# Optimization experiments

Hardware: AMD Instinct MI355X
Metric: run time of the kernel (lower is better)

## Reference

```python
import jax, jax.numpy as jnp
import numpy as np

B, N, F = 8, 1024, 64
H, C = 4, 32              # attention heads, channels per head
HIN = H * C               # GAT output size (concat heads) = 128
HID = 128                 # GRU hidden size
NEG_INF = -1e9


def _glorot(key, shape, fan_in, fan_out):
    scale = np.sqrt(2.0 / (fan_in + fan_out)).astype(np.float32)
    return jax.random.normal(key, shape, jnp.float32) * scale


def setup_inputs() -> dict:
    key = jax.random.key(0)
    ks = jax.random.split(key, 20)
    x = jax.random.normal(ks[0], (B, N, F), jnp.float32)
    a = (jax.random.uniform(ks[1], (B, N, N)) < 0.01).astype(jnp.float32)
    h = jax.random.normal(ks[2], (B, N, HID), jnp.float32) * 0.1
    # GATConv params (spektral dense mode, concat heads)
    Wk = _glorot(ks[3], (F, H, C), F, H * C)
    att_src = _glorot(ks[4], (H, C), C, 1)
    att_dst = _glorot(ks[5], (H, C), C, 1)
    bias_gat = jnp.zeros((HIN,), jnp.float32)
    # GRU-style gates (per-node biases, concat weights)
    b_u = _glorot(ks[6], (N, 1), N, 1)
    b_r = _glorot(ks[7], (N, 1), N, 1)
    b_c = _glorot(ks[8], (N, 1), N, 1)
    W_u = _glorot(ks[9], (HID + HIN, HID), HID + HIN, HID)
    W_r = _glorot(ks[10], (HID + HIN, HID), HID + HIN, HID)
    W_c = _glorot(ks[11], (HID + HIN, HID), HID + HIN, HID)
    # bilinear decoders
    R_p = _glorot(ks[12], (HID, HID), HID, HID)
    R_mu = _glorot(ks[13], (HID, HID), HID, HID)
    R_sigma = _glorot(ks[14], (HID, HID), HID, HID)
    return {"x": x, "a": a, "h": h, "Wk": Wk, "att_src": att_src,
            "att_dst": att_dst, "bias_gat": bias_gat,
            "b_u": b_u, "b_r": b_r, "b_c": b_c,
            "W_u": W_u, "W_r": W_r, "W_c": W_c,
            "R_p": R_p, "R_mu": R_mu, "R_sigma": R_sigma}


def reference(x, a, h, Wk, att_src, att_dst, bias_gat,
              b_u, b_r, b_c, W_u, W_r, W_c, R_p, R_mu, R_sigma):
    # ---- GATConv (dense mode, concat heads) ----
    hh = jnp.einsum('bnf,fhc->bnhc', x, Wk)                 # [B,N,H,C]
    s_src = jnp.einsum('bnhc,hc->bnh', hh, att_src)         # per-node src score
    s_dst = jnp.einsum('bnhc,hc->bnh', hh, att_dst)         # per-node dst score
    e = jax.nn.leaky_relu(s_src[:, :, None, :] + s_dst[:, None, :, :], 0.2)  # [B,N,N,H]
    e = e + NEG_INF * (1.0 - a)[..., None]                  # mask non-edges
    attn = jax.nn.softmax(e, axis=2)                        # softmax over neighbors j
    conv = jnp.einsum('bijh,bjhc->bihc', attn, hh)          # neighbor aggregation
    conv = conv.reshape(B, N, HIN) + bias_gat               # concat heads + bias
    # ---- GRU-style gated update ----
    cu = jnp.concatenate([conv, h], axis=-1)                # [B,N,HIN+HID]
    u = jax.nn.sigmoid(b_u + cu @ W_u)
    r = jax.nn.sigmoid(b_r + cu @ W_r)
    c = jnp.tanh(b_c + jnp.concatenate([conv, r * h], axis=-1) @ W_c)
    h_prime = u * h + (1.0 - u) * c                         # [B,N,HID]
    # dropout is identity at inference (training=False)
    # ---- three bilinear decoders ----
    def dec(R):
        return jnp.einsum('bnh,hk,bmk->bnm', h_prime, R, h_prime)
    logits = jnp.stack([dec(R_p), dec(R_mu), dec(R_sigma)], axis=-1)  # [B,N,N,3]
    return (logits, h_prime)
```

## Files before the change

kernel.cpp:

```cpp
#include <hip/hip_runtime.h>

#define BB 8
#define NNODES 1024
#define FIN 64
#define NH 4
#define NC 32
#define HDIM 128
#define NEG_INF_F (-1e9f)

#define LOGITS_CNT (BB*NNODES*NNODES*3)
#define HP_OFF LOGITS_CNT

#define CP1_OFF  (2*BB*NNODES*HDIM)
#define HHTB_OFF (3*BB*NNODES*HDIM)
#define WT_OFF   (4*BB*NNODES*HDIM)
#define RT_OFF   (WT_OFF + 49152)

#define WS_HH    0
#define WS_SSRC  (WS_HH    + BB*NNODES*HDIM)
#define WS_SDSTT (WS_SSRC  + BB*NNODES*NH)
#define WS_M     (WS_SDSTT + BB*NH*NNODES)
#define WS_RSUM  (WS_M     + BB*NNODES*NH)
#define WS_CONV  (WS_RSUM  + BB*NNODES*NH)
#define WS_T     (WS_CONV  + BB*NNODES*HDIM)
#define HPB_FOFF (WS_T + 1572864)

typedef float f32x4 __attribute__((ext_vector_type(4)));
typedef short bf16x8 __attribute__((ext_vector_type(8)));

__device__ __forceinline__ float sigmoidf_(float x) { return 1.0f/(1.0f+__expf(-x)); }
__device__ __forceinline__ float tanhf_(float x) {
  float e = __expf(2.0f*x); return 1.0f - 2.0f/(e+1.0f);
}
__device__ __forceinline__ void ld4(const float* p, float* d) {
  float4 v = *(const float4*)p;
  d[0]=v.x; d[1]=v.y; d[2]=v.z; d[3]=v.w;
}
__device__ __forceinline__ ushort f2b(float x) {
  union { float f; unsigned u; } v; v.f = x;
  unsigned r = v.u + 0x7fffu + ((v.u >> 16) & 1u);
  return (ushort)(r >> 16);
}

__global__ __launch_bounds__(256) void k_prep(
    const float* __restrict__ W_u, const float* __restrict__ W_r,
    const float* __restrict__ W_c, const float* __restrict__ R_p,
    const float* __restrict__ R_mu, const float* __restrict__ R_sg,
    float* __restrict__ out)
{
  __shared__ float tile[64*129];
  int blk = blockIdx.x, tid = threadIdx.x;
  const float* src; ushort* dst; int k0, nk;
  if (blk < 12) {
    int mat = blk >> 2, ch = blk & 3; k0 = ch*64; nk = 256;
    src = (mat==0) ? W_u : (mat==1) ? W_r : W_c;
    dst = (ushort*)(out + WT_OFF) + mat*32768;
  } else {
    int q = blk - 12; int mat = q >> 1, ch = q & 1; k0 = ch*64; nk = 128;
    src = (mat==0) ? R_p : (mat==1) ? R_mu : R_sg;
    dst = (ushort*)(out + RT_OFF) + mat*16384;
  }
  #pragma unroll
  for (int t = 0; t < 8; ++t) {
    int g = tid + t*256;
    int r = g >> 5, c4 = g & 31;
    *(float4*)&tile[r*129 + c4*4] = *(const float4*)&src[(size_t)(k0+r)*HDIM + c4*4];
  }
  __syncthreads();
  int c = tid >> 1, half = tid & 1;
  ushort tmp[32];
  #pragma unroll
  for (int q = 0; q < 32; ++q) tmp[q] = f2b(tile[(half*32+q)*129 + c]);
  size_t base = (size_t)c*nk + k0 + half*32;
  #pragma unroll
  for (int g = 0; g < 4; ++g) {
    uint4 v;
    v.x = (uint)tmp[g*8+0] | ((uint)tmp[g*8+1] << 16);
    v.y = (uint)tmp[g*8+2] | ((uint)tmp[g*8+3] << 16);
    v.z = (uint)tmp[g*8+4] | ((uint)tmp[g*8+5] << 16);
    v.w = (uint)tmp[g*8+6] | ((uint)tmp[g*8+7] << 16);
    *(uint4*)&dst[base + g*8] = v;
  }
}

#define XK_S 68
#define HT2_S 129
__global__ __launch_bounds__(256) void k_hh_scores(
    const float* __restrict__ x, const float* __restrict__ Wk,
    const float* __restrict__ att_src, const float* __restrict__ att_dst,
    float* __restrict__ ws, float* __restrict__ out)
{
  __shared__ union {
    struct { float wk[FIN*HDIM]; float x[32*XK_S]; } s;
    float hhT[32*HT2_S];
  } u;
  int tid = threadIdx.x;
  int blk = blockIdx.x;
  int b = blk >> 5;
  int n0 = (blk & 31) * 32;
  #pragma unroll
  for (int t = 0; t < 8; ++t) {
    int idx = tid + t*256;
    int r = idx >> 5, c4 = idx & 31;
    *(float4*)&u.s.wk[r*HDIM + c4*4] = *(const float4*)&Wk[r*HDIM + c4*4];
  }
  #pragma unroll
  for (int t = 0; t < 2; ++t) {
    int idx = tid + t*256;
    int r = idx >> 4, c4 = idx & 15;
    *(float4*)&u.s.x[r*XK_S + c4*4] =
      *(const float4*)&x[((size_t)(b*NNODES)+n0+r)*FIN + c4*4];
  }
  __syncthreads();
  int col = tid & 127;
  int rh = tid >> 7;
  float acc[16];
  #pragma unroll
  for (int rr = 0; rr < 16; ++rr) acc[rr] = 0.f;
  for (int k4 = 0; k4 < 16; ++k4) {
    float w0 = u.s.wk[(k4*4+0)*HDIM + col];
    float w1 = u.s.wk[(k4*4+1)*HDIM + col];
    float w2 = u.s.wk[(k4*4+2)*HDIM + col];
    float w3 = u.s.wk[(k4*4+3)*HDIM + col];
    #pragma unroll
    for (int rr = 0; rr < 16; ++rr) {
      float4 xv = *(const float4*)&u.s.x[(rh*16+rr)*XK_S + k4*4];
      acc[rr] = fmaf(xv.x, w0, fmaf(xv.y, w1, fmaf(xv.z, w2, fmaf(xv.w, w3, acc[rr]))));
    }
  }
  {
    float as = att_src[col], ad = att_dst[col];
    float* ssrc  = ws + WS_SSRC;
    float* sdstT = ws + WS_SDSTT;
    int hI = col >> 5;
    #pragma unroll
    for (int rr = 0; rr < 16; ++rr) {
      int n = n0 + rh*16 + rr;
      float ss = acc[rr]*as, sd = acc[rr]*ad;
      #pragma unroll
      for (int m = 16; m >= 1; m >>= 1) {
        ss += __shfl_xor(ss, m, 64);
        sd += __shfl_xor(sd, m, 64);
      }
      if ((col & 31) == 0) {
        ssrc[((size_t)(b*NNODES)+n)*NH + hI] = ss;
        sdstT[(size_t)(b*NH + hI)*NNODES + n] = sd;
      }
    }
  }
  __syncthreads();
  #pragma unroll
  for (int rr = 0; rr < 16; ++rr)
    u.hhT[(rh*16+rr)*HT2_S + col] = acc[rr];
  __syncthreads();
  {
    ushort* HHTB = (ushort*)(out + HHTB_OFF);
    int c = tid >> 1, half = tid & 1;
    ushort tmp[16];
    #pragma unroll
    for (int q = 0; q < 16; ++q)
      tmp[q] = f2b(u.hhT[(half*16+q)*HT2_S + c]);
    size_t base = ((size_t)(b*HDIM)+c)*NNODES + n0 + half*16;
    #pragma unroll
    for (int g = 0; g < 2; ++g) {
      uint4 v;
      v.x = (uint)tmp[g*8+0] | ((uint)tmp[g*8+1] << 16);
      v.y = (uint)tmp[g*8+2] | ((uint)tmp[g*8+3] << 16);
      v.z = (uint)tmp[g*8+4] | ((uint)tmp[g*8+5] << 16);
      v.w = (uint)tmp[g*8+6] | ((uint)tmp[g*8+7] << 16);
      *(uint4*)&HHTB[base + g*8] = v;
    }
  }
}

__global__ __launch_bounds__(256) void k_stats(
    const float* __restrict__ a, float* __restrict__ ws)
{
  __shared__ float a_l[NNODES];
  int tid = threadIdx.x;
  int blk = blockIdx.x;
  int b = blk & 7, i = blk >> 3;
  const float* arow = a + ((size_t)(b*NNODES + i))*NNODES;
  *(float4*)&a_l[tid*4] = *(const float4*)&arow[tid*4];
  __syncthreads();
  int h = tid >> 6, lane = tid & 63;
  const float* ssrc  = ws + WS_SSRC;
  const float* sdstT = ws + WS_SDSTT;
  float si = ssrc[((size_t)(b*NNODES)+i)*NH + h];
  float e[16];
  float mx = -3.4e38f;
  #pragma unroll
  for (int t = 0; t < 16; ++t) {
    int j = lane + t*64;
    float s = si + sdstT[(size_t)(b*NH+h)*NNODES + j];
    float ev = s >= 0.f ? s : 0.2f*s;
    ev += NEG_INF_F * (1.0f - a_l[j]);
    e[t] = ev;
    mx = fmaxf(mx, ev);
  }
  #pragma unroll
  for (int m = 32; m >= 1; m >>= 1) mx = fmaxf(mx, __shfl_xor(mx, m, 64));
  float sum = 0.f;
  #pragma unroll
  for (int t = 0; t < 16; ++t) sum += __expf(e[t] - mx);
  #pragma unroll
  for (int m = 32; m >= 1; m >>= 1) sum += __shfl_xor(sum, m, 64);
  if (lane == 0) {
    ws[WS_M    + ((size_t)(b*NNODES)+i)*NH + h] = mx;
    ws[WS_RSUM + ((size_t)(b*NNODES)+i)*NH + h] = 1.0f / sum;
  }
}

#define HT_S 40
__global__ __launch_bounds__(256) void k_conv_m(
    const float* __restrict__ a,
    float* __restrict__ ws, float* __restrict__ out)
{
  __shared__ ushort hhT_l[128*HT_S];
  __shared__ float sdst_l[4*32];
  int tid = threadIdx.x;
  int blk = blockIdx.x;
  int b = blk & 7;
  int rem = blk >> 3;
  int it = rem >> 1, jh = rem & 1;
  int i0 = it * 32;
  int j0b = jh * 512;
  int w = tid >> 6, lane = tid & 63;
  int i0w = i0 + (w & 1) * 16;
  int hp2 = (w >> 1) * 2;
  int i = i0w + (lane & 15);
  int koff = (lane >> 4) * 8;
  const ushort* HHTB = (const ushort*)(out + HHTB_OFF);
  const float* sdstT = ws + WS_SDSTT;
  float ssv[4], mv[4], rsv[4];
  ld4(&ws[WS_SSRC + ((size_t)(b*NNODES)+i)*4], ssv);
  ld4(&ws[WS_M    + ((size_t)(b*NNODES)+i)*4], mv);
  ld4(&ws[WS_RSUM + ((size_t)(b*NNODES)+i)*4], rsv);
  f32x4 acc[2][2];
  #pragma unroll
  for (int h = 0; h < 2; ++h)
    #pragma unroll
    for (int cf = 0; cf < 2; ++cf) acc[h][cf] = (f32x4)0.f;
  const float* arow = a + ((size_t)(b*NNODES)+i)*NNODES;
  for (int ch = 0; ch < 16; ++ch) {
    int j0 = j0b + ch*32;
    #pragma unroll
    for (int s = 0; s < 2; ++s) {
      int seg = tid + s*256;
      int c = seg >> 2, q = seg & 3;
      *(uint4*)&hhT_l[c*HT_S + q*8] =
        *(const uint4*)&HHTB[((size_t)(b*HDIM)+c)*NNODES + j0 + q*8];
    }
    if (tid < 32) {
      int h = tid >> 3, q = tid & 7;
      *(float4*)&sdst_l[h*32 + q*4] =
        *(const float4*)&sdstT[(size_t)(b*NH + h)*NNODES + j0 + q*4];
    }
    float av[8];
    {
      float4 a0 = *(const float4*)&arow[j0 + koff];
      float4 a1 = *(const float4*)&arow[j0 + koff + 4];
      av[0]=a0.x; av[1]=a0.y; av[2]=a0.z; av[3]=a0.w;
      av[4]=a1.x; av[5]=a1.y; av[6]=a1.z; av[7]=a1.w;
    }
    __syncthreads();
    float am[8];
    #pragma unroll
    for (int t = 0; t < 8; ++t) am[t] = fmaf(av[t], 1e9f, -1e9f);
    #pragma unroll
    for (int h2 = 0; h2 < 2; ++h2) {
      int hh_ = hp2 + h2;
      float sd[8];
      ld4(&sdst_l[hh_*32 + koff], sd);
      ld4(&sdst_l[hh_*32 + koff + 4], sd + 4);
      bf16x8 pf;
      #pragma unroll
      for (int t = 0; t < 8; ++t) {
        float s = ssv[hh_] + sd[t];
        s = fmaxf(s, 0.2f*s);
        float p = __expf(s + am[t] - mv[hh_]) * rsv[hh_];
        pf[t] = (short)f2b(p);
      }
      #pragma unroll
      for (int cf = 0; cf < 2; ++cf) {
        int c = hh_*32 + cf*16 + (lane & 15);
        bf16x8 bfr = *(const bf16x8*)&hhT_l[c*HT_S + koff];
        acc[h2][cf] = __builtin_amdgcn_mfma_f32_16x16x32_bf16(
            pf, bfr, acc[h2][cf], 0, 0, 0);
      }
    }
    __syncthreads();
  }
  float* cp = jh ? (out + CP1_OFF) : (ws + WS_CONV);
  int crow = (lane >> 4) * 4, ccol = lane & 15;
  #pragma unroll
  for (int h2 = 0; h2 < 2; ++h2)
    #pragma unroll
    for (int cf = 0; cf < 2; ++cf)
      #pragma unroll
      for (int r = 0; r < 4; ++r)
        cp[((size_t)(b*NNODES) + i0w + crow + r)*HDIM + (hp2+h2)*32 + cf*16 + ccol]
          = acc[h2][cf][r];
}

#define CU_S 264
#define RH_S 136
__global__ __launch_bounds__(256) void k_fuse(
    const float* __restrict__ h_in,
    const float* __restrict__ b_u, const float* __restrict__ b_r,
    const float* __restrict__ b_c, const float* __restrict__ bias_gat,
    float* __restrict__ ws, float* __restrict__ out)
{
  __shared__ ushort cu_l[16*CU_S];
  __shared__ ushort rh_l[16*RH_S];
  __shared__ ushort hp_l[16*RH_S];
  int tid = threadIdx.x;
  int blk = blockIdx.x;
  int b = blk & 7;
  int n0 = (blk >> 3) * 16;
  const float* conv0 = ws + WS_CONV;
  const float* conv1 = out + CP1_OFF;
  const ushort* WT = (const ushort*)(out + WT_OFF);
  const ushort* RT = (const ushort*)(out + RT_OFF);
  ushort* HPB = (ushort*)(ws + HPB_FOFF);
  ushort* TB  = (ushort*)(ws + WS_T);
  #pragma unroll
  for (int t = 0; t < 4; ++t) {
    int g = tid + t*256;
    int row = g >> 6, c4 = g & 63;
    float v[4];
    if (c4 < 32) {
      float4 v0 = *(const float4*)&conv0[((size_t)(b*NNODES)+n0+row)*HDIM + c4*4];
      float4 v1 = *(const float4*)&conv1[((size_t)(b*NNODES)+n0+row)*HDIM + c4*4];
      float4 bv = *(const float4*)&bias_gat[c4*4];
      v[0]=v0.x+v1.x+bv.x; v[1]=v0.y+v1.y+bv.y; v[2]=v0.z+v1.z+bv.z; v[3]=v0.w+v1.w+bv.w;
    } else {
      ld4(&h_in[((size_t)(b*NNODES)+n0+row)*HDIM + (c4-32)*4], v);
    }
    ushort4 o; o.x=f2b(v[0]); o.y=f2b(v[1]); o.z=f2b(v[2]); o.w=f2b(v[3]);
    *(ushort4*)&cu_l[row*CU_S + c4*4] = o;
  }
  __syncthreads();
  int w = tid >> 6, lane = tid & 63;
  int wn = w * 32;
  int fr = lane & 15, k8 = (lane >> 4) * 8;
  int crow = (lane >> 4) * 4, ccol = lane & 15;
  f32x4 acc_u[2], acc_r[2];
  acc_u[0]=(f32x4)0.f; acc_u[1]=(f32x4)0.f; acc_r[0]=(f32x4)0.f; acc_r[1]=(f32x4)0.f;
  #pragma unroll
  for (int ks = 0; ks < 8; ++ks) {
    bf16x8 afr = *(const bf16x8*)&cu_l[fr*CU_S + ks*32 + k8];
    #pragma unroll
    for (int nn = 0; nn < 2; ++nn) {
      int row = wn + nn*16 + fr;
      bf16x8 bu_ = *(const bf16x8*)&WT[(size_t)row*256 + ks*32 + k8];
      bf16x8 br_ = *(const bf16x8*)&WT[32768 + (size_t)row*256 + ks*32 + k8];
      acc_u[nn] = __builtin_amdgcn_mfma_f32_16x16x32_bf16(afr, bu_, acc_u[nn], 0,0,0);
      acc_r[nn] = __builtin_amdgcn_mfma_f32_16x16x32_bf16(afr, br_, acc_r[nn], 0,0,0);
    }
  }
  float u_reg[2][4], hv[2][4];
  float bu4[4], br4[4], bc4[4];
  #pragma unroll
  for (int r = 0; r < 4; ++r) {
    bu4[r] = b_u[n0 + crow + r];
    br4[r] = b_r[n0 + crow + r];
    bc4[r] = b_c[n0 + crow + r];
  }
  #pragma unroll
  for (int nn = 0; nn < 2; ++nn) {
    int col = wn + nn*16 + ccol;
    #pragma unroll
    for (int r = 0; r < 4; ++r) {
      int rown = crow + r;
      float h_ = h_in[((size_t)(b*NNODES)+n0+rown)*HDIM + col];
      hv[nn][r] = h_;
      u_reg[nn][r] = sigmoidf_(bu4[r] + acc_u[nn][r]);
      float rr_ = sigmoidf_(br4[r] + acc_r[nn][r]);
      rh_l[rown*RH_S + col] = f2b(rr_ * h_);
    }
  }
  __syncthreads();
  f32x4 acc_c[2];
  acc_c[0]=(f32x4)0.f; acc_c[1]=(f32x4)0.f;
  #pragma unroll
  for (int ks = 0; ks < 8; ++ks) {
    bf16x8 afr = (ks < 4)
      ? *(const bf16x8*)&cu_l[fr*CU_S + ks*32 + k8]
      : *(const bf16x8*)&rh_l[fr*RH_S + (ks-4)*32 + k8];
    #pragma unroll
    for (int nn = 0; nn < 2; ++nn) {
      int row = wn + nn*16 + fr;
      bf16x8 bc_ = *(const bf16x8*)&WT[65536 + (size_t)row*256 + ks*32 + k8];
      acc_c[nn] = __builtin_amdgcn_mfma_f32_16x16x32_bf16(afr, bc_, acc_c[nn], 0,0,0);
    }
  }
  #pragma unroll
  for (int nn = 0; nn < 2; ++nn) {
    int col = wn + nn*16 + ccol;
    #pragma unroll
    for (int r = 0; r < 4; ++r) {
      int rown = crow + r;
      float cc = tanhf_(bc4[r] + acc_c[nn][r]);
      float u_ = u_reg[nn][r];
      float hp = u_*hv[nn][r] + (1.0f-u_)*cc;
      out[HP_OFF + ((size_t)(b*NNODES)+n0+rown)*HDIM + col] = hp;
      ushort hb = f2b(hp);
      HPB[((size_t)(b*NNODES)+n0+rown)*HDIM + col] = hb;
      hp_l[rown*RH_S + col] = hb;
    }
  }
  __syncthreads();
  #pragma unroll
  for (int k3 = 0; k3 < 3; ++k3) {
    f32x4 acc_t[2];
    acc_t[0]=(f32x4)0.f; acc_t[1]=(f32x4)0.f;
    #pragma unroll
    for (int ks = 0; ks < 4; ++ks) {
      bf16x8 afr = *(const bf16x8*)&hp_l[fr*RH_S + ks*32 + k8];
      #pragma unroll
      for (int nn = 0; nn < 2; ++nn) {
        int row = wn + nn*16 + fr;
        bf16x8 bfr = *(const bf16x8*)&RT[k3*16384 + (size_t)row*128 + ks*32 + k8];
        acc_t[nn] = __builtin_amdgcn_mfma_f32_16x16x32_bf16(afr, bfr, acc_t[nn], 0,0,0);
      }
    }
    #pragma unroll
    for (int nn = 0; nn < 2; ++nn) {
      int col = wn + nn*16 + ccol;
      #pragma unroll
      for (int r = 0; r < 4; ++r)
        TB[((size_t)((b*3+k3)*NNODES)+n0+crow+r)*HDIM + col] = f2b(acc_t[nn][r]);
    }
  }
}

#define LT_S 136
__global__ __launch_bounds__(256) void k_logits_m(
    const float* __restrict__ ws, float* __restrict__ out)
{
  __shared__ ushort t_b[3][64*LT_S];
  __shared__ ushort hp_b[64*LT_S];
  const ushort* TB  = (const ushort*)(ws + WS_T);
  const ushort* HPB = (const ushort*)(ws + HPB_FOFF);
  int tid = threadIdx.x;
  int blk = blockIdx.x;
  int b = blk & 7;
  int rem = blk >> 3;
  int nt = rem >> 4, mt = rem & 15;
  int n0 = nt*64, m0 = mt*64;
  #pragma unroll
  for (int t = 0; t < 4; ++t) {
    int idx = tid + t*256;
    int r = idx >> 4, c = idx & 15;
    *(uint4*)&hp_b[r*LT_S + c*8] =
      *(const uint4*)&HPB[((size_t)(b*NNODES)+m0+r)*HDIM + c*8];
  }
  #pragma unroll
  for (int t = 0; t < 12; ++t) {
    int idx = tid + t*256;
    int k3 = idx >> 10, r = (idx >> 4) & 63, c = idx & 15;
    *(uint4*)&t_b[k3][r*LT_S + c*8] =
      *(const uint4*)&TB[((size_t)((b*3+k3)*NNODES)+n0+r)*HDIM + c*8];
  }
  __syncthreads();
  int w = tid >> 6, lane = tid & 63;
  int nbase = (w >> 1) * 32, mbase = (w & 1) * 32;
  int frow = lane & 15, fk = (lane >> 4) * 8;
  f32x4 acc[3][2][2];
  #pragma unroll
  for (int k3 = 0; k3 < 3; ++k3)
    #pragma unroll
    for (int nn = 0; nn < 2; ++nn)
      #pragma unroll
      for (int mm = 0; mm < 2; ++mm) acc[k3][nn][mm] = (f32x4)0.f;
  #pragma unroll
  for (int ks = 0; ks < 4; ++ks) {
    int ko = ks*32 + fk;
    bf16x8 bfr[2];
    #pragma unroll
    for (int mm = 0; mm < 2; ++mm)
      bfr[mm] = *(const bf16x8*)&hp_b[(mbase + mm*16 + frow)*LT_S + ko];
    #pragma unroll
    for (int k3 = 0; k3 < 3; ++k3)
      #pragma unroll
      for (int nn = 0; nn < 2; ++nn) {
        bf16x8 afr = *(const bf16x8*)&t_b[k3][(nbase + nn*16 + frow)*LT_S + ko];
        #pragma unroll
        for (int mm = 0; mm < 2; ++mm)
          acc[k3][nn][mm] = __builtin_amdgcn_mfma_f32_16x16x32_bf16(
              afr, bfr[mm], acc[k3][nn][mm], 0, 0, 0);
      }
  }
  int crow = (lane >> 4) * 4, ccol = lane & 15;
  #pragma unroll
  for (int nn = 0; nn < 2; ++nn)
    #pragma unroll
    for (int mm = 0; mm < 2; ++mm)
      #pragma unroll
      for (int r = 0; r < 4; ++r) {
        int n = n0 + nbase + nn*16 + crow + r;
        int m = m0 + mbase + mm*16 + ccol;
        float* po = &out[(((size_t)(b*NNODES) + n)*NNODES + m)*3];
        po[0] = acc[0][nn][mm][r];
        po[1] = acc[1][nn][mm][r];
        po[2] = acc[2][nn][mm][r];
      }
}

extern "C" void kernel_launch(void* const* d_in, const int* in_sizes, int n_in,
                              void* d_out, int out_size, void* d_ws, size_t ws_size,
                              hipStream_t stream) {
  (void)in_sizes; (void)n_in; (void)out_size; (void)ws_size;
  const float* x        = (const float*)d_in[0];
  const float* a        = (const float*)d_in[1];
  const float* h        = (const float*)d_in[2];
  const float* Wk       = (const float*)d_in[3];
  const float* att_src  = (const float*)d_in[4];
  const float* att_dst  = (const float*)d_in[5];
  const float* bias_gat = (const float*)d_in[6];
  const float* b_u      = (const float*)d_in[7];
  const float* b_r      = (const float*)d_in[8];
  const float* b_c      = (const float*)d_in[9];
  const float* W_u      = (const float*)d_in[10];
  const float* W_r      = (const float*)d_in[11];
  const float* W_c      = (const float*)d_in[12];
  const float* R_p      = (const float*)d_in[13];
  const float* R_mu     = (const float*)d_in[14];
  const float* R_sg     = (const float*)d_in[15];
  float* out = (float*)d_out;
  float* ws  = (float*)d_ws;

  hipLaunchKernelGGL(k_prep, dim3(18), dim3(256), 0, stream,
                     W_u, W_r, W_c, R_p, R_mu, R_sg, out);
  hipLaunchKernelGGL(k_hh_scores, dim3(256), dim3(256), 0, stream,
                     x, Wk, att_src, att_dst, ws, out);
  hipLaunchKernelGGL(k_stats, dim3(8192), dim3(256), 0, stream, a, ws);
  hipLaunchKernelGGL(k_conv_m, dim3(512), dim3(256), 0, stream, a, ws, out);
  hipLaunchKernelGGL(k_fuse, dim3(512), dim3(256), 0, stream,
                     h, b_u, b_r, b_c, bias_gat, ws, out);
  hipLaunchKernelGGL(k_logits_m, dim3(2048), dim3(256), 0, stream, ws, out);
}
```

Measured before the change: 100.7 us.

## Replace separate softmax stats pass with online softmax in conv kernel

Removes the k_stats kernel, which re-read the full adjacency matrix to compute per-row max and sum. k_conv_m now keeps a running max and sum per half of the neighbours (flash-attention style) and rescales its accumulators. k_fuse merges the two halves using the stored stats. The weight prep and hh/score kernels are also merged into one launch. This cuts a full pass over the adjacency and one launch, at the cost of extra exp, shuffles and rescaling inside the conv loop.

```diff
diff --git a/kernel.cpp b/kernel.cpp
--- a/kernel.cpp
+++ b/kernel.cpp
@@ -17,6 +17,8 @@
 #define RT_OFF   (WT_OFF + 49152)
 
 #define WS_HH    0
+#define WS_STATM WS_HH
+#define WS_STATS (WS_HH + 65536)
 #define WS_SSRC  (WS_HH    + BB*NNODES*HDIM)
 #define WS_SDSTT (WS_SSRC  + BB*NNODES*NH)
 #define WS_M     (WS_SDSTT + BB*NH*NNODES)
@@ -42,73 +44,70 @@
   return (ushort)(r >> 16);
 }
 
-__global__ __launch_bounds__(256) void k_prep(
+#define XK_S 68
+#define HT2_S 129
+__global__ __launch_bounds__(256) void k_pre(
+    const float* __restrict__ x, const float* __restrict__ Wk,
+    const float* __restrict__ att_src, const float* __restrict__ att_dst,
     const float* __restrict__ W_u, const float* __restrict__ W_r,
     const float* __restrict__ W_c, const float* __restrict__ R_p,
     const float* __restrict__ R_mu, const float* __restrict__ R_sg,
-    float* __restrict__ out)
-{
-  __shared__ float tile[64*129];
-  int blk = blockIdx.x, tid = threadIdx.x;
-  const float* src; ushort* dst; int k0, nk;
-  if (blk < 12) {
-    int mat = blk >> 2, ch = blk & 3; k0 = ch*64; nk = 256;
-    src = (mat==0) ? W_u : (mat==1) ? W_r : W_c;
-    dst = (ushort*)(out + WT_OFF) + mat*32768;
-  } else {
-    int q = blk - 12; int mat = q >> 1, ch = q & 1; k0 = ch*64; nk = 128;
-    src = (mat==0) ? R_p : (mat==1) ? R_mu : R_sg;
-    dst = (ushort*)(out + RT_OFF) + mat*16384;
-  }
-  #pragma unroll
-  for (int t = 0; t < 8; ++t) {
-    int g = tid + t*256;
-    int r = g >> 5, c4 = g & 31;
-    *(float4*)&tile[r*129 + c4*4] = *(const float4*)&src[(size_t)(k0+r)*HDIM + c4*4];
-  }
-  __syncthreads();
-  int c = tid >> 1, half = tid & 1;
-  ushort tmp[32];
-  #pragma unroll
-  for (int q = 0; q < 32; ++q) tmp[q] = f2b(tile[(half*32+q)*129 + c]);
-  size_t base = (size_t)c*nk + k0 + half*32;
-  #pragma unroll
-  for (int g = 0; g < 4; ++g) {
-    uint4 v;
-    v.x = (uint)tmp[g*8+0] | ((uint)tmp[g*8+1] << 16);
-    v.y = (uint)tmp[g*8+2] | ((uint)tmp[g*8+3] << 16);
-    v.z = (uint)tmp[g*8+4] | ((uint)tmp[g*8+5] << 16);
-    v.w = (uint)tmp[g*8+6] | ((uint)tmp[g*8+7] << 16);
-    *(uint4*)&dst[base + g*8] = v;
-  }
-}
-
-#define XK_S 68
-#define HT2_S 129
-__global__ __launch_bounds__(256) void k_hh_scores(
-    const float* __restrict__ x, const float* __restrict__ Wk,
-    const float* __restrict__ att_src, const float* __restrict__ att_dst,
     float* __restrict__ ws, float* __restrict__ out)
 {
-  __shared__ union {
-    struct { float wk[FIN*HDIM]; float x[32*XK_S]; } s;
-    float hhT[32*HT2_S];
-  } u;
-  int tid = threadIdx.x;
-  int blk = blockIdx.x;
-  int b = blk >> 5;
-  int n0 = (blk & 31) * 32;
+  __shared__ float sm[FIN*HDIM + 32*XK_S];
+  int blk = blockIdx.x, tid = threadIdx.x;
+  if (blk < 18) {
+    float* tile = sm;
+    const float* src; ushort* dst; int k0, nk;
+    if (blk < 12) {
+      int mat = blk >> 2, ch = blk & 3; k0 = ch*64; nk = 256;
+      src = (mat==0) ? W_u : (mat==1) ? W_r : W_c;
+      dst = (ushort*)(out + WT_OFF) + mat*32768;
+    } else {
+      int q = blk - 12; int mat = q >> 1, ch = q & 1; k0 = ch*64; nk = 128;
+      src = (mat==0) ? R_p : (mat==1) ? R_mu : R_sg;
+      dst = (ushort*)(out + RT_OFF) + mat*16384;
+    }
+    #pragma unroll
+    for (int t = 0; t < 8; ++t) {
+      int g = tid + t*256;
+      int r = g >> 5, c4 = g & 31;
+      *(float4*)&tile[r*129 + c4*4] = *(const float4*)&src[(size_t)(k0+r)*HDIM + c4*4];
+    }
+    __syncthreads();
+    int c = tid >> 1, half = tid & 1;
+    ushort tmp[32];
+    #pragma unroll
+    for (int q = 0; q < 32; ++q) tmp[q] = f2b(tile[(half*32+q)*129 + c]);
+    size_t base = (size_t)c*nk + k0 + half*32;
+    #pragma unroll
+    for (int g = 0; g < 4; ++g) {
+      uint4 v;
+      v.x = (uint)tmp[g*8+0] | ((uint)tmp[g*8+1] << 16);
+      v.y = (uint)tmp[g*8+2] | ((uint)tmp[g*8+3] << 16);
+      v.z = (uint)tmp[g*8+4] | ((uint)tmp[g*8+5] << 16);
+      v.w = (uint)tmp[g*8+6] | ((uint)tmp[g*8+7] << 16);
+      *(uint4*)&dst[base + g*8] = v;
+    }
+    return;
+  }
+  int blk2 = blk - 18;
+  int b = blk2 >> 5;
+  int n0 = (blk2 & 31) * 32;
+  float* wk_l = sm;
+  float* x_l  = sm + FIN*HDIM;
+  float* hhT  = sm;
   #pragma unroll
   for (int t = 0; t < 8; ++t) {
     int idx = tid + t*256;
     int r = idx >> 5, c4 = idx & 31;
-    *(float4*)&u.s.wk[r*HDIM + c4*4] = *(const float4*)&Wk[r*HDIM + c4*4];
+    *(float4*)&wk_l[r*HDIM + c4*4] = *(const float4*)&Wk[r*HDIM + c4*4];
   }
   #pragma unroll
   for (int t = 0; t < 2; ++t) {
     int idx = tid + t*256;
     int r = idx >> 4, c4 = idx & 15;
-    *(float4*)&u.s.x[r*XK_S + c4*4] =
+    *(float4*)&x_l[r*XK_S + c4*4] =
       *(const float4*)&x[((size_t)(b*NNODES)+n0+r)*FIN + c4*4];
   }
   __syncthreads();
@@ -118,13 +117,13 @@
   #pragma unroll
   for (int rr = 0; rr < 16; ++rr) acc[rr] = 0.f;
   for (int k4 = 0; k4 < 16; ++k4) {
-    float w0 = u.s.wk[(k4*4+0)*HDIM + col];
-    float w1 = u.s.wk[(k4*4+1)*HDIM + col];
-    float w2 = u.s.wk[(k4*4+2)*HDIM + col];
-    float w3 = u.s.wk[(k4*4+3)*HDIM + col];
+    float w0 = wk_l[(k4*4+0)*HDIM + col];
+    float w1 = wk_l[(k4*4+1)*HDIM + col];
+    float w2 = wk_l[(k4*4+2)*HDIM + col];
+    float w3 = wk_l[(k4*4+3)*HDIM + col];
     #pragma unroll
     for (int rr = 0; rr < 16; ++rr) {
-      float4 xv = *(const float4*)&u.s.x[(rh*16+rr)*XK_S + k4*4];
+      float4 xv = *(const float4*)&x_l[(rh*16+rr)*XK_S + k4*4];
       acc[rr] = fmaf(xv.x, w0, fmaf(xv.y, w1, fmaf(xv.z, w2, fmaf(xv.w, w3, acc[rr]))));
     }
   }
@@ -151,7 +150,7 @@
   __syncthreads();
   #pragma unroll
   for (int rr = 0; rr < 16; ++rr)
-    u.hhT[(rh*16+rr)*HT2_S + col] = acc[rr];
+    hhT[(rh*16+rr)*HT2_S + col] = acc[rr];
   __syncthreads();
   {
     ushort* HHTB = (ushort*)(out + HHTB_OFF);
@@ -159,7 +158,7 @@
     ushort tmp[16];
     #pragma unroll
     for (int q = 0; q < 16; ++q)
-      tmp[q] = f2b(u.hhT[(half*16+q)*HT2_S + c]);
+      tmp[q] = f2b(hhT[(half*16+q)*HT2_S + c]);
     size_t base = ((size_t)(b*HDIM)+c)*NNODES + n0 + half*16;
     #pragma unroll
     for (int g = 0; g < 2; ++g) {
@@ -170,44 +169,6 @@
       v.w = (uint)tmp[g*8+6] | ((uint)tmp[g*8+7] << 16);
       *(uint4*)&HHTB[base + g*8] = v;
     }
-  }
-}
-
-__global__ __launch_bounds__(256) void k_stats(
-    const float* __restrict__ a, float* __restrict__ ws)
-{
-  __shared__ float a_l[NNODES];
-  int tid = threadIdx.x;
-  int blk = blockIdx.x;
-  int b = blk & 7, i = blk >> 3;
-  const float* arow = a + ((size_t)(b*NNODES + i))*NNODES;
-  *(float4*)&a_l[tid*4] = *(const float4*)&arow[tid*4];
-  __syncthreads();
-  int h = tid >> 6, lane = tid & 63;
-  const float* ssrc  = ws + WS_SSRC;
-  const float* sdstT = ws + WS_SDSTT;
-  float si = ssrc[((size_t)(b*NNODES)+i)*NH + h];
-  float e[16];
-  float mx = -3.4e38f;
-  #pragma unroll
-  for (int t = 0; t < 16; ++t) {
-    int j = lane + t*64;
-    float s = si + sdstT[(size_t)(b*NH+h)*NNODES + j];
-    float ev = s >= 0.f ? s : 0.2f*s;
-    ev += NEG_INF_F * (1.0f - a_l[j]);
-    e[t] = ev;
-    mx = fmaxf(mx, ev);
-  }
-  #pragma unroll
-  for (int m = 32; m >= 1; m >>= 1) mx = fmaxf(mx, __shfl_xor(mx, m, 64));
-  float sum = 0.f;
-  #pragma unroll
-  for (int t = 0; t < 16; ++t) sum += __expf(e[t] - mx);
-  #pragma unroll
-  for (int m = 32; m >= 1; m >>= 1) sum += __shfl_xor(sum, m, 64);
-  if (lane == 0) {
-    ws[WS_M    + ((size_t)(b*NNODES)+i)*NH + h] = mx;
-    ws[WS_RSUM + ((size_t)(b*NNODES)+i)*NH + h] = 1.0f / sum;
   }
 }
 
@@ -228,14 +189,16 @@
   int w = tid >> 6, lane = tid & 63;
   int i0w = i0 + (w & 1) * 16;
   int hp2 = (w >> 1) * 2;
-  int i = i0w + (lane & 15);
+  int fr = lane & 15;
+  int i = i0w + fr;
   int koff = (lane >> 4) * 8;
+  int crow = (lane >> 4) * 4, ccol = lane & 15;
   const ushort* HHTB = (const ushort*)(out + HHTB_OFF);
   const float* sdstT = ws + WS_SDSTT;
-  float ssv[4], mv[4], rsv[4];
+  float ssv[4];
   ld4(&ws[WS_SSRC + ((size_t)(b*NNODES)+i)*4], ssv);
-  ld4(&ws[WS_M    + ((size_t)(b*NNODES)+i)*4], mv);
-  ld4(&ws[WS_RSUM + ((size_t)(b*NNODES)+i)*4], rsv);
+  float m_run[2] = {-3.0e38f, -3.0e38f};
+  float s_run[2] = {0.f, 0.f};
   f32x4 acc[2][2];
   #pragma unroll
   for (int h = 0; h < 2; ++h)
@@ -273,16 +236,38 @@
       float sd[8];
       ld4(&sdst_l[hh_*32 + koff], sd);
       ld4(&sdst_l[hh_*32 + koff + 4], sd + 4);
-      bf16x8 pf;
+      float e[8];
+      float mx = -3.0e38f;
       #pragma unroll
       for (int t = 0; t < 8; ++t) {
         float s = ssv[hh_] + sd[t];
         s = fmaxf(s, 0.2f*s);
-        float p = __expf(s + am[t] - mv[hh_]) * rsv[hh_];
+        e[t] = s + am[t];
+        mx = fmaxf(mx, e[t]);
+      }
+      mx = fmaxf(mx, __shfl_xor(mx, 16, 64));
+      mx = fmaxf(mx, __shfl_xor(mx, 32, 64));
+      float mnew = fmaxf(m_run[h2], mx);
+      float scale = __expf(m_run[h2] - mnew);
+      bf16x8 pf;
+      float sum8 = 0.f;
+      #pragma unroll
+      for (int t = 0; t < 8; ++t) {
+        float p = __expf(e[t] - mnew);
+        sum8 += p;
         pf[t] = (short)f2b(p);
       }
+      sum8 += __shfl_xor(sum8, 16, 64);
+      sum8 += __shfl_xor(sum8, 32, 64);
+      s_run[h2] = s_run[h2]*scale + sum8;
+      m_run[h2] = mnew;
+      float sc[4];
+      #pragma unroll
+      for (int r = 0; r < 4; ++r) sc[r] = __shfl(scale, crow + r, 64);
       #pragma unroll
       for (int cf = 0; cf < 2; ++cf) {
+        #pragma unroll
+        for (int r = 0; r < 4; ++r) acc[h2][cf][r] *= sc[r];
         int c = hh_*32 + cf*16 + (lane & 15);
         bf16x8 bfr = *(const bf16x8*)&hhT_l[c*HT_S + koff];
         acc[h2][cf] = __builtin_amdgcn_mfma_f32_16x16x32_bf16(
@@ -292,7 +277,6 @@
     __syncthreads();
   }
   float* cp = jh ? (out + CP1_OFF) : (ws + WS_CONV);
-  int crow = (lane >> 4) * 4, ccol = lane & 15;
   #pragma unroll
   for (int h2 = 0; h2 < 2; ++h2)
     #pragma unroll
@@ -301,6 +285,13 @@
       for (int r = 0; r < 4; ++r)
         cp[((size_t)(b*NNODES) + i0w + crow + r)*HDIM + (hp2+h2)*32 + cf*16 + ccol]
           = acc[h2][cf][r];
+  if (lane < 16) {
+    size_t si = ((size_t)(b*NNODES) + i0w + lane)*NH;
+    ws[WS_STATM + jh*32768 + si + hp2]     = m_run[0];
+    ws[WS_STATM + jh*32768 + si + hp2 + 1] = m_run[1];
+    ws[WS_STATS + jh*32768 + si + hp2]     = s_run[0];
+    ws[WS_STATS + jh*32768 + si + hp2 + 1] = s_run[1];
+  }
 }
 
 #define CU_S 264
@@ -330,10 +321,19 @@
     int row = g >> 6, c4 = g & 63;
     float v[4];
     if (c4 < 32) {
+      int hh_ = c4 >> 3;
+      size_t sidx = ((size_t)(b*NNODES)+n0+row)*NH + hh_;
+      float m0 = ws[WS_STATM + sidx], m1 = ws[WS_STATM + 32768 + sidx];
+      float s0 = ws[WS_STATS + sidx], s1 = ws[WS_STATS + 32768 + sidx];
+      float M = fmaxf(m0, m1);
+      float f0 = __expf(m0 - M), f1 = __expf(m1 - M);
+      float rd = 1.0f / (s0*f0 + s1*f1);
+      f0 *= rd; f1 *= rd;
       float4 v0 = *(const float4*)&conv0[((size_t)(b*NNODES)+n0+row)*HDIM + c4*4];
       float4 v1 = *(const float4*)&conv1[((size_t)(b*NNODES)+n0+row)*HDIM + c4*4];
       float4 bv = *(const float4*)&bias_gat[c4*4];
-      v[0]=v0.x+v1.x+bv.x; v[1]=v0.y+v1.y+bv.y; v[2]=v0.z+v1.z+bv.z; v[3]=v0.w+v1.w+bv.w;
+      v[0]=v0.x*f0+v1.x*f1+bv.x; v[1]=v0.y*f0+v1.y*f1+bv.y;
+      v[2]=v0.z*f0+v1.z*f1+bv.z; v[3]=v0.w*f0+v1.w*f1+bv.w;
     } else {
       ld4(&h_in[((size_t)(b*NNODES)+n0+row)*HDIM + (c4-32)*4], v);
     }
@@ -531,11 +531,8 @@
   float* out = (float*)d_out;
   float* ws  = (float*)d_ws;
 
-  hipLaunchKernelGGL(k_prep, dim3(18), dim3(256), 0, stream,
-                     W_u, W_r, W_c, R_p, R_mu, R_sg, out);
-  hipLaunchKernelGGL(k_hh_scores, dim3(256), dim3(256), 0, stream,
-                     x, Wk, att_src, att_dst, ws, out);
-  hipLaunchKernelGGL(k_stats, dim3(8192), dim3(256), 0, stream, a, ws);
+  hipLaunchKernelGGL(k_pre, dim3(274), dim3(256), 0, stream,
+                     x, Wk, att_src, att_dst, W_u, W_r, W_c, R_p, R_mu, R_sg, ws, out);
   hipLaunchKernelGGL(k_conv_m, dim3(512), dim3(256), 0, stream, a, ws, out);
   hipLaunchKernelGGL(k_fuse, dim3(512), dim3(256), 0, stream,
                      h, b_u, b_r, b_c, bias_gat, ws, out);
```

Measured after the change: 90.51 us. -10.1%, faster.
